# Kernel tuning notes

Hardware: AMD Instinct MI355X
Metric: run time of the kernel (lower is better)

## Reference

```python
import jax, jax.numpy as jnp
import numpy as np


def setup_inputs() -> dict:
    key = jax.random.key(0)
    ks = jax.random.split(key, 6)
    B, L, C = 32, 336, 512
    t = L // 2 + 1  # 169 rfft frequencies; four_l must equal t
    s = 1.0 / np.sqrt(C)
    return {
        "x": jax.random.normal(ks[0], (B, L, C), jnp.float32),
        "Wr": jax.random.normal(ks[1], (t, C, C), jnp.float32) * s,  # real part of complex Linear weights [t, out, in]
        "Wi": jax.random.normal(ks[2], (t, C, C), jnp.float32) * s,  # imag part
        "br": jax.random.normal(ks[3], (t, C), jnp.float32) * s,
        "bi": jax.random.normal(ks[4], (t, C), jnp.float32) * s,
        "weights": jax.random.normal(ks[5], (t,), jnp.float32),
    }


def reference(x, Wr, Wi, br, bi, weights):
    # x: [B, L, C] real. rfft along time with ortho norm -> [B, t, C] complex.
    B, L, C = x.shape
    t = Wr.shape[0]
    n = 2 * (t - 1)  # torch irfft default output length (== L, L even)
    xf = jnp.fft.rfft(x, axis=1, norm='ortho')  # [B, t, C] complex64

    # Per-frequency complex linear: y[b,i,o] = sum_c xf[b,i,c] * W[i,o,c] + b[i,o].
    # This fuses the original repeat + eye-mask + python loop into one batched GEMM.
    W = Wr + 1j * Wi
    b = br + 1j * bi
    y = jnp.einsum('bic,ioc->bio', xf, W) + b[None]  # [B, t, C]

    # The original builds fre[b,i,:,c] as a spectrum that is one-hot at frequency i
    # (value y[b,i,c]) and irffts along the frequency axis (ortho norm). For a one-hot
    # spectrum: irfft(onehot_i * y)[l] = scale_i * Re(y * exp(2*pi*j*i*l/n)) / sqrt(n),
    # with scale_i = 2 except at DC (i=0) and Nyquist (i=t-1) where it is 1
    # (imag parts of DC/Nyquist bins are discarded by C2R, matching torch).
    # Finally ConcatenationWithLearnableCoefficient sums over i with softmax weights,
    # so we fold softmax(weights) * scale_i / sqrt(n) into one coefficient per i.
    i_idx = jnp.arange(t)
    scale = jnp.where((i_idx == 0) | (i_idx == t - 1), 1.0, 2.0).astype(jnp.float32)
    w = jax.nn.softmax(weights)
    coef = w * scale / jnp.sqrt(jnp.float32(n))  # [t]

    l_idx = jnp.arange(n)
    theta = (2.0 * jnp.pi / n) * (i_idx[:, None] * l_idx[None, :]).astype(jnp.float32)  # [t, n]
    cos_m, sin_m = jnp.cos(theta), jnp.sin(theta)

    yr = y.real * coef[None, :, None]
    yi = y.imag * coef[None, :, None]
    # Re(y * e^{j theta}) = yr*cos - yi*sin ; sum over frequencies i -> [B, n, C]
    out = jnp.einsum('bic,il->blc', yr, cos_m) - jnp.einsum('bic,il->blc', yi, sin_m)
    return out
```

## Files before the change

### kernel.cpp

```cpp
#include <hip/hip_runtime.h>
#include <math.h>

typedef short   s16x8  __attribute__((ext_vector_type(8)));
typedef __bf16  bf16x8 __attribute__((ext_vector_type(8)));
typedef float   f32x4  __attribute__((ext_vector_type(4)));

#define T_FREQ 169
#define NN     336
#define CCH    512
#define BB     32
#define TP     176
#define LP     352
#define KP     192

static constexpr size_t OFF_COEF = 0;
static constexpr size_t OFF_FC   = 1024;
static constexpr size_t OFF_FS   = OFF_FC + 124928;
static constexpr size_t OFF_CCOS = OFF_FS + 124928;
static constexpr size_t OFF_CSIN = OFF_CCOS + 130048;
static constexpr size_t OFF_XT   = OFF_CSIN + 130048;
static constexpr size_t OFF_XR   = OFF_XT + (size_t)BB*CCH*LP*2;
static constexpr size_t OFF_XI   = OFF_XR + (size_t)TP*BB*CCH*2;
static constexpr size_t OFF_YR   = OFF_XI + (size_t)TP*BB*CCH*2;
static constexpr size_t OFF_YI   = OFF_YR + (size_t)BB*KP*CCH*2;

__device__ __forceinline__ unsigned short f2bf(float f){
  return __builtin_bit_cast(unsigned short, (__bf16)f);
}

__device__ __forceinline__ bf16x8 cvt8(float4 lo, float4 hi){
  bf16x8 r;
  r[0]=(__bf16)lo.x; r[1]=(__bf16)lo.y; r[2]=(__bf16)lo.z; r[3]=(__bf16)lo.w;
  r[4]=(__bf16)hi.x; r[5]=(__bf16)hi.y; r[6]=(__bf16)hi.z; r[7]=(__bf16)hi.w;
  return r;
}

__device__ __forceinline__ f32x4 mfma16(bf16x8 a, bf16x8 b, f32x4 c){
  return __builtin_amdgcn_mfma_f32_16x16x32_bf16(a, b, c, 0, 0, 0);
}

__global__ __launch_bounds__(256) void prep_tables(const float* __restrict__ wts, char* ws){
  float* coef = (float*)(ws + OFF_COEF);
  unsigned short* Fc  = (unsigned short*)(ws + OFF_FC);
  unsigned short* Fs  = (unsigned short*)(ws + OFF_FS);
  unsigned short* Cc  = (unsigned short*)(ws + OFF_CCOS);
  unsigned short* Cs  = (unsigned short*)(ws + OFF_CSIN);
  const float PI2_N = 6.283185307179586f / (float)NN;
  const float inv_sqrt_n = 0.05455447255899809f;

  if (blockIdx.x == 0){
    __shared__ float red[256];
    int tid = threadIdx.x;
    float v = (tid < T_FREQ) ? wts[tid] : -1e30f;
    red[tid] = v; __syncthreads();
    for (int s = 128; s > 0; s >>= 1){ if (tid < s) red[tid] = fmaxf(red[tid], red[tid+s]); __syncthreads(); }
    float mx = red[0]; __syncthreads();
    float e = (tid < T_FREQ) ? expf(v - mx) : 0.f;
    red[tid] = e; __syncthreads();
    for (int s = 128; s > 0; s >>= 1){ if (tid < s) red[tid] += red[tid+s]; __syncthreads(); }
    float ssum = red[0];
    if (tid < T_FREQ){
      float sc = (tid == 0 || tid == T_FREQ-1) ? 1.f : 2.f;
      coef[tid] = (e / ssum) * sc * inv_sqrt_n;
    }
    return;
  }
  int gid = (blockIdx.x - 1) * 256 + threadIdx.x;
  int stride = (gridDim.x - 1) * 256;
  for (int e = gid; e < TP*LP; e += stride){
    int i = e / LP, l = e % LP;
    float c = 0.f, s = 0.f;
    if (l < NN){
      int m = (i * l) % NN;
      float sv, cv; sincosf(PI2_N * (float)m, &sv, &cv);
      c = cv * inv_sqrt_n; s = -sv * inv_sqrt_n;
    }
    Fc[e] = f2bf(c); Fs[e] = f2bf(s);
  }
  for (int e = gid; e < NN*KP; e += stride){
    int l = e / KP, i = e % KP;
    float c = 0.f, s = 0.f;
    if (i < T_FREQ){
      int m = (i * l) % NN;
      float sv, cv; sincosf(PI2_N * (float)m, &sv, &cv);
      c = cv; s = -sv;
    }
    Cc[e] = f2bf(c); Cs[e] = f2bf(s);
  }
}

__global__ __launch_bounds__(256) void transpose_x(const float* __restrict__ x, char* ws){
  unsigned short* xt = (unsigned short*)(ws + OFF_XT);
  __shared__ float tile[32][33];
  int bid = blockIdx.x;
  int b  = bid / (11*16);
  int rm = bid % (11*16);
  int lt = rm / 16, ct = rm % 16;
  int tx = threadIdx.x & 31, ty = threadIdx.x >> 5;
  #pragma unroll
  for (int k = 0; k < 4; ++k){
    int l = lt*32 + ty + k*8;
    int c = ct*32 + tx;
    float v = (l < NN) ? x[((size_t)b*NN + l)*CCH + c] : 0.f;
    tile[ty + k*8][tx] = v;
  }
  __syncthreads();
  #pragma unroll
  for (int k = 0; k < 4; ++k){
    int crow = ct*32 + ty + k*8;
    int lcol = lt*32 + tx;
    xt[((size_t)b*CCH + crow)*LP + lcol] = f2bf(tile[tx][ty + k*8]);
  }
}

__global__ __launch_bounds__(256) void stage_rfft(char* ws){
  const unsigned short* xt = (const unsigned short*)(ws + OFF_XT);
  const unsigned short* Fc = (const unsigned short*)(ws + OFF_FC);
  const unsigned short* Fs = (const unsigned short*)(ws + OFF_FS);
  unsigned short* xr = (unsigned short*)(ws + OFF_XR);
  unsigned short* xi = (unsigned short*)(ws + OFF_XI);

  int bid = blockIdx.x;
  int b  = bid >> 4;
  int rm = bid & 15;
  int c0 = (rm & 7) * 64;
  int mh = rm >> 3;
  int mbase = mh * 5;
  int tid = threadIdx.x, lane = tid & 63, wv = tid >> 6;
  int kg = lane >> 4, ln = lane & 15;
  int c = c0 + wv*16 + ln;

  f32x4 aR[6], aI[6];
  #pragma unroll
  for (int m = 0; m < 6; ++m){ aR[m] = (f32x4){0,0,0,0}; aI[m] = (f32x4){0,0,0,0}; }

  const unsigned short* xrow = xt + ((size_t)b*CCH + c)*LP;
  for (int kk = 0; kk < 11; ++kk){
    int ko = kk*32 + kg*8;
    bf16x8 bx = *(const bf16x8*)(xrow + ko);
    #pragma unroll
    for (int m = 0; m < 6; ++m){
      bf16x8 fc = *(const bf16x8*)(Fc + (size_t)((mbase+m)*16 + ln)*LP + ko);
      bf16x8 fs = *(const bf16x8*)(Fs + (size_t)((mbase+m)*16 + ln)*LP + ko);
      aR[m] = mfma16(fc, bx, aR[m]);
      aI[m] = mfma16(fs, bx, aI[m]);
    }
  }
  int rbase = kg*4;
  #pragma unroll
  for (int m = 0; m < 6; ++m){
    #pragma unroll
    for (int r = 0; r < 4; ++r){
      int i = (mbase+m)*16 + rbase + r;
      size_t off = ((size_t)i*BB + b)*CCH + c;
      xr[off] = f2bf(aR[m][r]);
      xi[off] = f2bf(aI[m][r]);
    }
  }
}

__global__ __launch_bounds__(256, 4) void stage_cgemm(const float* __restrict__ Wr, const float* __restrict__ Wi,
                                                      const float* __restrict__ br, const float* __restrict__ bi,
                                                      char* ws){
  const unsigned short* xr = (const unsigned short*)(ws + OFF_XR);
  const unsigned short* xi = (const unsigned short*)(ws + OFF_XI);
  const float* coef = (const float*)(ws + OFF_COEF);
  unsigned short* yr = (unsigned short*)(ws + OFF_YR);
  unsigned short* yi = (unsigned short*)(ws + OFF_YI);

  __shared__ unsigned short sW[2][16*CCH];

  int bid = blockIdx.x;
  int i  = bid >> 5;
  int ot = bid & 31;
  int tid = threadIdx.x, lane = tid & 63, wv = tid >> 6;
  int kg = lane >> 4, ln = lane & 15;

  const float* gWr = Wr + ((size_t)i*CCH + ot*16)*CCH;
  const float* gWi = Wi + ((size_t)i*CCH + ot*16)*CCH;
  float4 buf[16];
  #pragma unroll
  for (int j = 0; j < 4; ++j){
    int row = j*4 + wv;
    const float* s = gWr + (size_t)row*CCH + lane*8;
    buf[2*j]   = *(const float4*)(s);
    buf[2*j+1] = *(const float4*)(s + 4);
  }
  #pragma unroll
  for (int j = 0; j < 4; ++j){
    int row = j*4 + wv;
    const float* s = gWi + (size_t)row*CCH + lane*8;
    buf[8+2*j]   = *(const float4*)(s);
    buf[8+2*j+1] = *(const float4*)(s + 4);
  }
  #pragma unroll
  for (int j = 0; j < 4; ++j){
    int row = j*4 + wv;
    int dst = row*CCH + ((lane ^ (row & 7)) << 3);
    *(bf16x8*)&sW[0][dst] = cvt8(buf[2*j],   buf[2*j+1]);
    *(bf16x8*)&sW[1][dst] = cvt8(buf[8+2*j], buf[8+2*j+1]);
  }
  __syncthreads();

  int mb = wv & 1, part = wv >> 1;
  f32x4 acc = (f32x4){0,0,0,0};
  const unsigned short* xa = xr + (size_t)(i*BB + mb*16 + ln)*CCH;
  const unsigned short* xb = xi + (size_t)(i*BB + mb*16 + ln)*CCH;

  #pragma unroll
  for (int kk = 0; kk < 16; ++kk){
    int ko = kk*32 + kg*8;
    bf16x8 ar = *(const bf16x8*)(xa + ko);
    bf16x8 ai = *(const bf16x8*)(xb + ko);
    int g = (((kk*4 + kg) ^ (ln & 7)) << 3);
    bf16x8 wr8 = *(const bf16x8*)&sW[0][ln*CCH + g];
    bf16x8 wi8 = *(const bf16x8*)&sW[1][ln*CCH + g];
    bf16x8 nwi = __builtin_bit_cast(bf16x8, (s16x8)(__builtin_bit_cast(s16x8, wi8) ^ (short)0x8000));
    bf16x8 b1 = part ? wi8 : wr8;
    bf16x8 b2 = part ? wr8 : nwi;
    acc = mfma16(ar, b1, acc);
    acc = mfma16(ai, b2, acc);
  }

  int o = ot*16 + ln;
  float cf = coef[i];
  float bias = (part ? bi : br)[(size_t)i*CCH + o];
  unsigned short* yp = part ? yi : yr;
  #pragma unroll
  for (int r = 0; r < 4; ++r){
    int bb = mb*16 + kg*4 + r;
    yp[((size_t)bb*KP + i)*CCH + o] = f2bf((acc[r] + bias) * cf);
  }
}

__global__ __launch_bounds__(256) void stage_irfft(const char* ws_c, float* __restrict__ out){
  const char* ws = ws_c;
  const unsigned short* Cc = (const unsigned short*)(ws + OFF_CCOS);
  const unsigned short* Cs = (const unsigned short*)(ws + OFF_CSIN);
  const unsigned short* yr = (const unsigned short*)(ws + OFF_YR);
  const unsigned short* yi = (const unsigned short*)(ws + OFF_YI);

  __shared__ unsigned short lr[64][40];
  __shared__ unsigned short li[64][40];

  int bid = blockIdx.x;
  int b  = bid >> 4;
  int rm = bid & 15;
  int c0 = (rm & 7) * 64;
  int mh = rm >> 3;
  int mbase = mh * 10;
  int tid = threadIdx.x, lane = tid & 63, wv = tid >> 6;
  int kg = lane >> 4, ln = lane & 15;

  f32x4 acc[11];
  #pragma unroll
  for (int m = 0; m < 11; ++m) acc[m] = (f32x4){0,0,0,0};

  for (int kk = 0; kk < 6; ++kk){
    if (kk) __syncthreads();
    #pragma unroll
    for (int q = 0; q < 8; ++q){
      int idx = q*256 + tid;
      int ir = idx >> 6, cc = idx & 63;
      int i = kk*32 + ir;
      unsigned short vr = 0, vi = 0;
      if (i < T_FREQ){
        size_t off = ((size_t)b*KP + i)*CCH + c0 + cc;
        vr = yr[off]; vi = yi[off];
      }
      lr[cc][ir] = vr;
      li[cc][ir] = vi;
    }
    __syncthreads();
    int ko = kk*32 + kg*8;
    bf16x8 blr = *(const bf16x8*)(&lr[wv*16 + ln][kg*8]);
    bf16x8 bli = *(const bf16x8*)(&li[wv*16 + ln][kg*8]);
    #pragma unroll
    for (int m = 0; m < 11; ++m){
      bf16x8 ac = *(const bf16x8*)(Cc + (size_t)((mbase+m)*16 + ln)*KP + ko);
      bf16x8 as = *(const bf16x8*)(Cs + (size_t)((mbase+m)*16 + ln)*KP + ko);
      acc[m] = mfma16(ac, blr, acc[m]);
      acc[m] = mfma16(as, bli, acc[m]);
    }
  }

  int cdst = c0 + wv*16 + ln;
  #pragma unroll
  for (int m = 0; m < 11; ++m){
    #pragma unroll
    for (int r = 0; r < 4; ++r){
      int l = (mbase+m)*16 + kg*4 + r;
      out[((size_t)b*NN + l)*CCH + cdst] = acc[m][r];
    }
  }
}

extern "C" void kernel_launch(void* const* d_in, const int* in_sizes, int n_in,
                              void* d_out, int out_size, void* d_ws, size_t ws_size,
                              hipStream_t stream){
  const float* x   = (const float*)d_in[0];
  const float* Wr  = (const float*)d_in[1];
  const float* Wi  = (const float*)d_in[2];
  const float* br  = (const float*)d_in[3];
  const float* bi  = (const float*)d_in[4];
  const float* wts = (const float*)d_in[5];
  char* ws = (char*)d_ws;

  prep_tables<<<257, 256, 0, stream>>>(wts, ws);
  transpose_x<<<32*11*16, 256, 0, stream>>>(x, ws);
  stage_rfft<<<512, 256, 0, stream>>>(ws);
  stage_cgemm<<<T_FREQ*32, 256, 0, stream>>>(Wr, Wi, br, bi, ws);
  stage_irfft<<<512, 256, 0, stream>>>(ws, (float*)d_out);
}
```

Before: 201.8 us.

## Stream complex GEMM weights via async global-to-LDS loads with double buffering

The complex GEMM stage now copies the fp32 weight tiles straight from global memory into LDS with global_load_lds, in four K-chunks of 128, double-buffered so the next chunk's load overlaps MFMA work on the current one. The bf16 conversion moves from a single up-front staging pass to the inner loop, reading swizzled fp32 values from LDS. This removes the register staging buffer and the serialized load-then-compute prologue, and the occupancy hint rises from 4 to 5 blocks. In exchange each weight element is converted once per wave instead of once per block, LDS reads double because fp32 is read instead of bf16, and each chunk now ends with an extra barrier.

```diff
diff --git a/kernel.cpp b/kernel.cpp
--- a/kernel.cpp
+++ b/kernel.cpp
@@ -12,6 +12,7 @@
 #define TP     176
 #define LP     352
 #define KP     192
+#define QK     128
 
 static constexpr size_t OFF_COEF = 0;
 static constexpr size_t OFF_FC   = 1024;
@@ -35,8 +36,21 @@
   return r;
 }
 
+__device__ __forceinline__ bf16x8 cvt8v(f32x4 lo, f32x4 hi){
+  bf16x8 r;
+  r[0]=(__bf16)lo[0]; r[1]=(__bf16)lo[1]; r[2]=(__bf16)lo[2]; r[3]=(__bf16)lo[3];
+  r[4]=(__bf16)hi[0]; r[5]=(__bf16)hi[1]; r[6]=(__bf16)hi[2]; r[7]=(__bf16)hi[3];
+  return r;
+}
+
 __device__ __forceinline__ f32x4 mfma16(bf16x8 a, bf16x8 b, f32x4 c){
   return __builtin_amdgcn_mfma_f32_16x16x32_bf16(a, b, c, 0, 0, 0);
+}
+
+typedef __attribute__((address_space(3))) unsigned lds_u32;
+typedef __attribute__((address_space(1))) const unsigned g_u32;
+__device__ __forceinline__ void gll16(const void* g, void* l){
+  __builtin_amdgcn_global_load_lds((g_u32*)g, (lds_u32*)l, 16, 0, 0);
 }
 
 __global__ __launch_bounds__(256) void prep_tables(const float* __restrict__ wts, char* ws){
@@ -159,7 +173,7 @@
   }
 }
 
-__global__ __launch_bounds__(256, 4) void stage_cgemm(const float* __restrict__ Wr, const float* __restrict__ Wi,
+__global__ __launch_bounds__(256, 5) void stage_cgemm(const float* __restrict__ Wr, const float* __restrict__ Wi,
                                                       const float* __restrict__ br, const float* __restrict__ bi,
                                                       char* ws){
   const unsigned short* xr = (const unsigned short*)(ws + OFF_XR);
@@ -168,7 +182,7 @@
   unsigned short* yr = (unsigned short*)(ws + OFF_YR);
   unsigned short* yi = (unsigned short*)(ws + OFF_YI);
 
-  __shared__ unsigned short sW[2][16*CCH];
+  __shared__ float sW[2][2][16][QK];
 
   int bid = blockIdx.x;
   int i  = bid >> 5;
@@ -176,31 +190,20 @@
   int tid = threadIdx.x, lane = tid & 63, wv = tid >> 6;
   int kg = lane >> 4, ln = lane & 15;
 
-  const float* gWr = Wr + ((size_t)i*CCH + ot*16)*CCH;
-  const float* gWi = Wi + ((size_t)i*CCH + ot*16)*CCH;
-  float4 buf[16];
+  const float* gsrc[4];
+  float* ldst0[4];
+  float* ldst1[4];
   #pragma unroll
   for (int j = 0; j < 4; ++j){
-    int row = j*4 + wv;
-    const float* s = gWr + (size_t)row*CCH + lane*8;
-    buf[2*j]   = *(const float4*)(s);
-    buf[2*j+1] = *(const float4*)(s + 4);
-  }
-  #pragma unroll
-  for (int j = 0; j < 4; ++j){
-    int row = j*4 + wv;
-    const float* s = gWi + (size_t)row*CCH + lane*8;
-    buf[8+2*j]   = *(const float4*)(s);
-    buf[8+2*j+1] = *(const float4*)(s + 4);
-  }
-  #pragma unroll
-  for (int j = 0; j < 4; ++j){
-    int row = j*4 + wv;
-    int dst = row*CCH + ((lane ^ (row & 7)) << 3);
-    *(bf16x8*)&sW[0][dst] = cvt8(buf[2*j],   buf[2*j+1]);
-    *(bf16x8*)&sW[1][dst] = cvt8(buf[8+2*j], buf[8+2*j+1]);
-  }
-  __syncthreads();
+    int c = wv*4 + j;
+    int p = c >> 3;
+    int r = ((c & 7) << 1) + (lane >> 5);
+    int G = (lane & 31) ^ (r & 7);
+    const float* base = p ? Wi : Wr;
+    gsrc[j] = base + ((size_t)i*CCH + ot*16 + r)*CCH + G*4;
+    ldst0[j] = &sW[0][p][(c & 7) << 1][0];
+    ldst1[j] = &sW[1][p][(c & 7) << 1][0];
+  }
 
   int mb = wv & 1, part = wv >> 1;
   f32x4 acc = (f32x4){0,0,0,0};
@@ -208,18 +211,43 @@
   const unsigned short* xb = xi + (size_t)(i*BB + mb*16 + ln)*CCH;
 
   #pragma unroll
-  for (int kk = 0; kk < 16; ++kk){
-    int ko = kk*32 + kg*8;
-    bf16x8 ar = *(const bf16x8*)(xa + ko);
-    bf16x8 ai = *(const bf16x8*)(xb + ko);
-    int g = (((kk*4 + kg) ^ (ln & 7)) << 3);
-    bf16x8 wr8 = *(const bf16x8*)&sW[0][ln*CCH + g];
-    bf16x8 wi8 = *(const bf16x8*)&sW[1][ln*CCH + g];
-    bf16x8 nwi = __builtin_bit_cast(bf16x8, (s16x8)(__builtin_bit_cast(s16x8, wi8) ^ (short)0x8000));
-    bf16x8 b1 = part ? wi8 : wr8;
-    bf16x8 b2 = part ? wr8 : nwi;
-    acc = mfma16(ar, b1, acc);
-    acc = mfma16(ai, b2, acc);
+  for (int j = 0; j < 4; ++j) gll16(gsrc[j], ldst0[j]);
+  asm volatile("s_waitcnt vmcnt(0)" ::: "memory");
+  __syncthreads();
+
+  #pragma unroll
+  for (int q = 0; q < 4; ++q){
+    const int cur = q & 1;
+    if (q < 3){
+      #pragma unroll
+      for (int j = 0; j < 4; ++j)
+        gll16(gsrc[j] + (size_t)(q+1)*QK, cur ? ldst0[j] : ldst1[j]);
+    }
+    const float* wr_row = &sW[cur][0][ln][0];
+    const float* wi_row = &sW[cur][1][ln][0];
+    #pragma unroll
+    for (int kkl = 0; kkl < 4; ++kkl){
+      int ko = q*QK + kkl*32 + kg*8;
+      bf16x8 ar = *(const bf16x8*)(xa + ko);
+      bf16x8 ai = *(const bf16x8*)(xb + ko);
+      int g0 = ((kkl*8 + kg*2 + 0) ^ (ln & 7)) * 4;
+      int g1 = ((kkl*8 + kg*2 + 1) ^ (ln & 7)) * 4;
+      f32x4 w0 = *(const f32x4*)(wr_row + g0);
+      f32x4 w1 = *(const f32x4*)(wr_row + g1);
+      f32x4 v0 = *(const f32x4*)(wi_row + g0);
+      f32x4 v1 = *(const f32x4*)(wi_row + g1);
+      bf16x8 wr8 = cvt8v(w0, w1);
+      bf16x8 wi8 = cvt8v(v0, v1);
+      bf16x8 nwi = __builtin_bit_cast(bf16x8, (s16x8)(__builtin_bit_cast(s16x8, wi8) ^ (short)0x8000));
+      bf16x8 b1 = part ? wi8 : wr8;
+      bf16x8 b2 = part ? wr8 : nwi;
+      acc = mfma16(ar, b1, acc);
+      acc = mfma16(ai, b2, acc);
+    }
+    if (q < 3){
+      asm volatile("s_waitcnt vmcnt(0)" ::: "memory");
+      __syncthreads();
+    }
   }
 
   int o = ot*16 + ln;
```

After: 195.9 us. 1.03x faster.

## Stream W tiles into LDS with async global_load_lds in four chunks

Applied to the files above, without the earlier changes.

The complex GEMM stage now loads the fp32 weight tile straight into shared memory using the async global-to-LDS load builtin, split into four K-chunks with staged vmcnt waits, so MFMA compute on early chunks overlaps the loads of later ones. The bf16 conversion moves from a register staging pass to the point of use after the LDS read. The X operands are preloaded into registers up front. This doubles the LDS footprint (fp32 rather than bf16) and raises register pressure, so launch bounds drop from 4 to 2 blocks per SM, which reduces occupancy.

```diff
diff --git a/kernel.cpp b/kernel.cpp
--- a/kernel.cpp
+++ b/kernel.cpp
@@ -12,6 +12,7 @@
 #define TP     176
 #define LP     352
 #define KP     192
+#define QK     128
 
 static constexpr size_t OFF_COEF = 0;
 static constexpr size_t OFF_FC   = 1024;
@@ -28,15 +29,21 @@
   return __builtin_bit_cast(unsigned short, (__bf16)f);
 }
 
-__device__ __forceinline__ bf16x8 cvt8(float4 lo, float4 hi){
+__device__ __forceinline__ bf16x8 cvt8v(f32x4 lo, f32x4 hi){
   bf16x8 r;
-  r[0]=(__bf16)lo.x; r[1]=(__bf16)lo.y; r[2]=(__bf16)lo.z; r[3]=(__bf16)lo.w;
-  r[4]=(__bf16)hi.x; r[5]=(__bf16)hi.y; r[6]=(__bf16)hi.z; r[7]=(__bf16)hi.w;
+  r[0]=(__bf16)lo[0]; r[1]=(__bf16)lo[1]; r[2]=(__bf16)lo[2]; r[3]=(__bf16)lo[3];
+  r[4]=(__bf16)hi[0]; r[5]=(__bf16)hi[1]; r[6]=(__bf16)hi[2]; r[7]=(__bf16)hi[3];
   return r;
 }
 
 __device__ __forceinline__ f32x4 mfma16(bf16x8 a, bf16x8 b, f32x4 c){
   return __builtin_amdgcn_mfma_f32_16x16x32_bf16(a, b, c, 0, 0, 0);
+}
+
+typedef __attribute__((address_space(3))) unsigned lds_u32;
+typedef __attribute__((address_space(1))) const unsigned g_u32;
+__device__ __forceinline__ void gll16(const void* g, void* l){
+  __builtin_amdgcn_global_load_lds((g_u32*)g, (lds_u32*)l, 16, 0, 0);
 }
 
 __global__ __launch_bounds__(256) void prep_tables(const float* __restrict__ wts, char* ws){
@@ -159,7 +166,33 @@
   }
 }
 
-__global__ __launch_bounds__(256, 4) void stage_cgemm(const float* __restrict__ Wr, const float* __restrict__ Wi,
+#define WAIT_BAR(N) \
+  asm volatile("s_waitcnt vmcnt(" #N ")" ::: "memory"); \
+  __builtin_amdgcn_s_barrier(); \
+  __builtin_amdgcn_sched_barrier(0)
+
+#define COMPUTE_CHUNK(C) do{ \
+  const float* wrr = &sW[C][0][ln][0]; \
+  const float* wir = &sW[C][1][ln][0]; \
+  _Pragma("unroll") \
+  for (int kkl = 0; kkl < 4; ++kkl){ \
+    int q0 = ((kkl*8 + kg*2 + 0) ^ ln7) << 2; \
+    int q1 = ((kkl*8 + kg*2 + 1) ^ ln7) << 2; \
+    f32x4 w0 = *(const f32x4*)(wrr + q0); \
+    f32x4 w1 = *(const f32x4*)(wrr + q1); \
+    f32x4 v0 = *(const f32x4*)(wir + q0); \
+    f32x4 v1 = *(const f32x4*)(wir + q1); \
+    bf16x8 wr8 = cvt8v(w0, w1); \
+    bf16x8 wi8 = cvt8v(v0, v1); \
+    bf16x8 nwi = __builtin_bit_cast(bf16x8, (s16x8)(__builtin_bit_cast(s16x8, wi8) ^ (short)0x8000)); \
+    bf16x8 b1 = part ? wi8 : wr8; \
+    bf16x8 b2 = part ? wr8 : nwi; \
+    acc = mfma16(xA[(C)*4 + kkl], b1, acc); \
+    acc = mfma16(xB[(C)*4 + kkl], b2, acc); \
+  } \
+}while(0)
+
+__global__ __launch_bounds__(256, 2) void stage_cgemm(const float* __restrict__ Wr, const float* __restrict__ Wi,
                                                       const float* __restrict__ br, const float* __restrict__ bi,
                                                       char* ws){
   const unsigned short* xr = (const unsigned short*)(ws + OFF_XR);
@@ -168,59 +201,49 @@
   unsigned short* yr = (unsigned short*)(ws + OFF_YR);
   unsigned short* yi = (unsigned short*)(ws + OFF_YI);
 
-  __shared__ unsigned short sW[2][16*CCH];
+  __shared__ float sW[4][2][16][QK];
 
   int bid = blockIdx.x;
   int i  = bid >> 5;
   int ot = bid & 31;
   int tid = threadIdx.x, lane = tid & 63, wv = tid >> 6;
-  int kg = lane >> 4, ln = lane & 15;
-
-  const float* gWr = Wr + ((size_t)i*CCH + ot*16)*CCH;
-  const float* gWi = Wi + ((size_t)i*CCH + ot*16)*CCH;
-  float4 buf[16];
-  #pragma unroll
-  for (int j = 0; j < 4; ++j){
-    int row = j*4 + wv;
-    const float* s = gWr + (size_t)row*CCH + lane*8;
-    buf[2*j]   = *(const float4*)(s);
-    buf[2*j+1] = *(const float4*)(s + 4);
-  }
-  #pragma unroll
-  for (int j = 0; j < 4; ++j){
-    int row = j*4 + wv;
-    const float* s = gWi + (size_t)row*CCH + lane*8;
-    buf[8+2*j]   = *(const float4*)(s);
-    buf[8+2*j+1] = *(const float4*)(s + 4);
-  }
-  #pragma unroll
-  for (int j = 0; j < 4; ++j){
-    int row = j*4 + wv;
-    int dst = row*CCH + ((lane ^ (row & 7)) << 3);
-    *(bf16x8*)&sW[0][dst] = cvt8(buf[2*j],   buf[2*j+1]);
-    *(bf16x8*)&sW[1][dst] = cvt8(buf[8+2*j], buf[8+2*j+1]);
-  }
-  __syncthreads();
-
+  int kg = lane >> 4, ln = lane & 15, ln7 = ln & 7;
   int mb = wv & 1, part = wv >> 1;
-  f32x4 acc = (f32x4){0,0,0,0};
+
   const unsigned short* xa = xr + (size_t)(i*BB + mb*16 + ln)*CCH;
   const unsigned short* xb = xi + (size_t)(i*BB + mb*16 + ln)*CCH;
-
+  bf16x8 xA[16], xB[16];
   #pragma unroll
   for (int kk = 0; kk < 16; ++kk){
     int ko = kk*32 + kg*8;
-    bf16x8 ar = *(const bf16x8*)(xa + ko);
-    bf16x8 ai = *(const bf16x8*)(xb + ko);
-    int g = (((kk*4 + kg) ^ (ln & 7)) << 3);
-    bf16x8 wr8 = *(const bf16x8*)&sW[0][ln*CCH + g];
-    bf16x8 wi8 = *(const bf16x8*)&sW[1][ln*CCH + g];
-    bf16x8 nwi = __builtin_bit_cast(bf16x8, (s16x8)(__builtin_bit_cast(s16x8, wi8) ^ (short)0x8000));
-    bf16x8 b1 = part ? wi8 : wr8;
-    bf16x8 b2 = part ? wr8 : nwi;
-    acc = mfma16(ar, b1, acc);
-    acc = mfma16(ai, b2, acc);
-  }
+    xA[kk] = *(const bf16x8*)(xa + ko);
+    xB[kk] = *(const bf16x8*)(xb + ko);
+  }
+  __builtin_amdgcn_sched_barrier(0);
+
+  {
+    const float* wbase = (wv >> 1) ? Wi : Wr;
+    const float* gW = wbase + ((size_t)i*CCH + ot*16)*CCH;
+    int rl = lane >> 5, g = lane & 31;
+    #pragma unroll
+    for (int c = 0; c < 4; ++c){
+      #pragma unroll
+      for (int j = 0; j < 4; ++j){
+        int rb = (wv & 1)*8 + j*2;
+        int r  = rb + rl;
+        int G  = g ^ (r & 7);
+        gll16(gW + (size_t)r*CCH + c*QK + G*4, &sW[c][wv>>1][rb][0]);
+      }
+      __builtin_amdgcn_sched_barrier(0);
+    }
+  }
+
+  f32x4 acc = (f32x4){0,0,0,0};
+
+  WAIT_BAR(12); COMPUTE_CHUNK(0);
+  WAIT_BAR(8);  COMPUTE_CHUNK(1);
+  WAIT_BAR(4);  COMPUTE_CHUNK(2);
+  WAIT_BAR(0);  COMPUTE_CHUNK(3);
 
   int o = ot*16 + ln;
   float cf = coef[i];
```

New measurement: 210.5 us. 4.3% more time.
